# Performance work log

Hardware: AMD Instinct MI355X
Metric: run time of the kernel (lower is better)

## Reference

```python
import jax, jax.numpy as jnp
import numpy as np

EPS = 1e-5

def _bn(x, g, b, m, v):
    # eval-mode batchnorm, NCHW, per-channel params
    inv = g / jnp.sqrt(v + EPS)
    return x * inv[None, :, None, None] + (b - m * inv)[None, :, None, None]

def setup_inputs() -> dict:
    key = jax.random.key(0)
    ks = jax.random.split(key, 16)
    C = 64
    x = jax.random.normal(ks[0], (8, C, 64, 64), dtype=jnp.float32)
    w1 = jax.random.normal(ks[1], (C, C, 1, 1), dtype=jnp.float32) * 0.1
    w2 = jax.random.normal(ks[2], (C, 1, 3, 3), dtype=jnp.float32) * 0.1
    w3 = jax.random.normal(ks[3], (C, C, 1, 1), dtype=jnp.float32) * 0.1
    def bn_params(k):
        k1, k2, k3, k4 = jax.random.split(k, 4)
        return (jax.random.uniform(k1, (C,)) + 0.5,
                jax.random.normal(k2, (C,)) * 0.1,
                jax.random.normal(k3, (C,)) * 0.1,
                jax.random.uniform(k4, (C,)) + 0.5)
    g1, b1, m1, v1 = bn_params(ks[4])
    g2, b2, m2, v2 = bn_params(ks[5])
    g3, b3, m3, v3 = bn_params(ks[6])
    return {"x": x, "w1": w1, "bn1_g": g1, "bn1_b": b1, "bn1_m": m1, "bn1_v": v1,
            "w2": w2, "bn2_g": g2, "bn2_b": b2, "bn2_m": m2, "bn2_v": v2,
            "w3": w3, "bn3_g": g3, "bn3_b": b3, "bn3_m": m3, "bn3_v": v3}

def reference(x, w1, bn1_g, bn1_b, bn1_m, bn1_v,
              w2, bn2_g, bn2_b, bn2_m, bn2_v,
              w3, bn3_g, bn3_b, bn3_m, bn3_v):
    B, c, h, w = x.shape
    N = h * w
    # conv1 (1x1) + BN + ReLU -> V
    v = jnp.einsum('bchw,oc->bohw', x, w1[:, :, 0, 0])
    v = jax.nn.relu(_bn(v, bn1_g, bn1_b, bn1_m, bn1_v))
    # attention over spatial positions: Q=K=x, single head, dim=c
    Q = x.reshape(B, c, N)          # bdn
    V = v.reshape(B, c, N)          # bdm
    scores = jnp.einsum('bdn,bdm->bnm', Q, Q) / (c ** 0.5)  # [B,N,N]
    prob = jax.nn.softmax(scores, axis=-1)
    out = jnp.einsum('bnm,bdm->bdn', prob, V).reshape(B, c, h, w)
    # depthwise conv + BN + ReLU
    out = jax.lax.conv_general_dilated(
        out, w2, window_strides=(1, 1), padding='SAME',
        dimension_numbers=('NCHW', 'OIHW', 'NCHW'), feature_group_count=c)
    out = jax.nn.relu(_bn(out, bn2_g, bn2_b, bn2_m, bn2_v))
    # pointwise conv + BN
    out = jnp.einsum('bchw,oc->bohw', out, w3[:, :, 0, 0])
    out = _bn(out, bn3_g, bn3_b, bn3_m, bn3_v)
    # residual (stride==1 and in_size==out_size)
    return out + x
```

## Files before the change

kernel.cpp:

```cpp
#include <hip/hip_runtime.h>
#include <stdint.h>

typedef __attribute__((ext_vector_type(8)))  short s16x8;
typedef __attribute__((ext_vector_type(16))) float f32x16;

union CvtI4 { int4 i; s16x8 s; };

__device__ __forceinline__ unsigned f2bf(float f) {
    union { float f; unsigned u; } v; v.f = f;
    return (v.u + 0x7fffu + ((v.u >> 16) & 1u)) >> 16;
}

__global__ __launch_bounds__(256) void k_prep(
    const float* __restrict__ x, const float* __restrict__ w1,
    const float* __restrict__ g1, const float* __restrict__ b1,
    const float* __restrict__ m1, const float* __restrict__ v1,
    unsigned short* __restrict__ xT, unsigned short* __restrict__ vbf)
{
    __shared__ float X[64 * 65];
    const int b    = blockIdx.x >> 7;
    const int n0   = ((blockIdx.x >> 1) & 63) << 6;
    const int half = blockIdx.x & 1;
    const int tid  = threadIdx.x;
    const float QS = 0.42466090014400953f;

    {
        const int r = tid >> 6, nn = tid & 63;
        const float* xb = x + (size_t)b * 262144 + n0 + nn;
#pragma unroll
        for (int cc = 0; cc < 16; ++cc) {
            int c = cc * 4 + r;
            X[c * 65 + nn] = xb[(size_t)c * 4096];
        }
    }
    __syncthreads();

    {
        const int n8 = tid >> 3, c8 = tid & 7;
        const int n = (half << 5) + n8;
        unsigned u[4];
#pragma unroll
        for (int j = 0; j < 4; ++j) {
            unsigned lo = f2bf(X[(c8 * 8 + 2 * j) * 65 + n] * QS);
            unsigned hi = f2bf(X[(c8 * 8 + 2 * j + 1) * 65 + n] * QS);
            u[j] = lo | (hi << 16);
        }
        uint4 pk; pk.x = u[0]; pk.y = u[1]; pk.z = u[2]; pk.w = u[3];
        *(uint4*)(xT + (((size_t)((b << 12) + n0 + n)) << 6) + (c8 << 3)) = pk;
    }

    {
        const int n = tid & 63, og = tid >> 6;
        float rX[64];
#pragma unroll
        for (int c = 0; c < 64; ++c) rX[c] = X[c * 65 + n];
        unsigned short* vb = vbf + (((size_t)(b << 6)) << 12) + n0 + n;
#pragma unroll 2
        for (int oo = 0; oo < 8; ++oo) {
            int o = (half << 5) + og * 8 + oo;
            float inv = g1[o] * rsqrtf(v1[o] + 1e-5f);
            float sh  = b1[o] - m1[o] * inv;
            float acc = 0.f;
#pragma unroll
            for (int c = 0; c < 64; ++c) acc = fmaf(w1[o * 64 + c], rX[c], acc);
            vb[(size_t)o << 12] = (unsigned short)f2bf(fmaxf(fmaf(acc, inv, sh), 0.f));
        }
    }
}

__global__ __launch_bounds__(256) void k_attn(
    const unsigned short* __restrict__ xT, const unsigned short* __restrict__ vbf,
    unsigned short* __restrict__ outO, float* __restrict__ outL,
    int tilesPer, int nsplit)
{
    __shared__ __align__(16) unsigned short Klds[64 * 64];
    __shared__ __align__(16) unsigned short Vlds[64 * 64];
    __shared__ __align__(16) unsigned short Plds[64 * 64];
    __shared__ float rsLds[4][32];
    __shared__ float denomT[64];

    const int xcd  = blockIdx.x & 7;
    const int slot = blockIdx.x >> 3;
    const int qgrp = slot & 63;
    const int pair = xcd * nsplit + (slot >> 6);
    const int b = pair & 7;
    const int ms = pair >> 3;

    const int tid = threadIdx.x;
    const int w = tid >> 6, lane = tid & 63;
    const int l31 = lane & 31, half = lane >> 5;
    const int qbase = qgrp << 6;

    outO += (size_t)ms * 2097152u;
    outL += (size_t)ms * 32768u;

    const int s = w & 1;
    const int t = w >> 1;

    s16x8 Bq[4];
    {
        const unsigned short* qr = xT +
            (((size_t)((b << 12) + qbase + (t << 5) + l31)) << 6) + (half << 3);
#pragma unroll
        for (int kk = 0; kk < 4; ++kk) {
            CvtI4 c; c.i = *(const int4*)(qr + (kk << 4));
            Bq[kk] = c.s;
        }
    }

    f32x16 O = {0.f,0.f,0.f,0.f,0.f,0.f,0.f,0.f,0.f,0.f,0.f,0.f,0.f,0.f,0.f,0.f};
    float rs = 0.f;
    const int mt0 = ms * tilesPer;

    for (int mt = 0; mt < tilesPer; ++mt) {
        const int m0 = (mt0 + mt) << 6;
        __syncthreads();
#pragma unroll
        for (int it = 0; it < 2; ++it) {
            int lin = (it << 8) + tid;
            {
                int km = lin >> 3, c4 = lin & 7;
                int4 d = *(const int4*)(xT + (((size_t)((b << 12) + m0 + km)) << 6) + (c4 << 3));
                *(int4*)(Klds + (km << 6) + ((c4 ^ (km & 7)) << 3)) = d;
            }
            {
                int vd = lin >> 3, c8 = lin & 7;
                int4 d = *(const int4*)(vbf + (((size_t)((b << 6) + vd)) << 12) + m0 + (c8 << 3));
                *(int4*)(Vlds + (vd << 6) + ((c8 ^ (vd & 7)) << 3)) = d;
            }
        }
        __syncthreads();

        {
            const int km = (s << 5) + l31;
            s16x8 Ak[4];
#pragma unroll
            for (int kk = 0; kk < 4; ++kk) {
                int pos = ((kk << 1) + half) ^ (km & 7);
                Ak[kk] = *(const s16x8*)(Klds + (km << 6) + (pos << 3));
            }
            f32x16 S = {0.f,0.f,0.f,0.f,0.f,0.f,0.f,0.f,0.f,0.f,0.f,0.f,0.f,0.f,0.f,0.f};
            S = __builtin_amdgcn_mfma_f32_32x32x16_bf16(Ak[0], Bq[0], S, 0, 0, 0);
            S = __builtin_amdgcn_mfma_f32_32x32x16_bf16(Ak[1], Bq[1], S, 0, 0, 0);
            S = __builtin_amdgcn_mfma_f32_32x32x16_bf16(Ak[2], Bq[2], S, 0, 0, 0);
            S = __builtin_amdgcn_mfma_f32_32x32x16_bf16(Ak[3], Bq[3], S, 0, 0, 0);

            const int nrow = (t << 5) + l31;
#pragma unroll
            for (int q = 0; q < 4; ++q) {
                float p0 = __builtin_amdgcn_exp2f(S[4*q+0]);
                float p1 = __builtin_amdgcn_exp2f(S[4*q+1]);
                float p2 = __builtin_amdgcn_exp2f(S[4*q+2]);
                float p3 = __builtin_amdgcn_exp2f(S[4*q+3]);
                rs += (p0 + p1) + (p2 + p3);
                union { float f; unsigned u; } a0, a1, a2, a3;
                a0.f = p0; a1.f = p1; a2.f = p2; a3.f = p3;
                uint2 pk;
                pk.x = ((a0.u + 0x8000u) >> 16) | ((a1.u + 0x8000u) & 0xFFFF0000u);
                pk.y = ((a2.u + 0x8000u) >> 16) | ((a3.u + 0x8000u) & 0xFFFF0000u);
                int c8 = (s << 2) + q;
                *(uint2*)(Plds + (nrow << 6) + ((c8 ^ (nrow & 7)) << 3) + (half << 2)) = pk;
            }
        }
        __syncthreads();

        {
            const int nrow = (t << 5) + l31;
            const int drow = (s << 5) + l31;
#pragma unroll
            for (int ks = 0; ks < 4; ++ks) {
                int c = (ks << 1) + half;
                const s16x8 Ap = *(const s16x8*)(Plds + (nrow << 6) + ((c ^ (nrow & 7)) << 3));
                const s16x8 Bv = *(const s16x8*)(Vlds + (drow << 6) + ((c ^ (drow & 7)) << 3));
                O = __builtin_amdgcn_mfma_f32_32x32x16_bf16(Ap, Bv, O, 0, 0, 0);
            }
        }
    }

    rs += __shfl_xor(rs, 32);
    if (half == 0) rsLds[w][l31] = rs;
    __syncthreads();
    if (tid < 64) {
        int tt = tid >> 5, n = tid & 31;
        denomT[tid] = rsLds[2 * tt][n] + rsLds[2 * tt + 1][n];
    }
    __syncthreads();

    const int nb = (b << 12) + qbase;
    const int n32o = w >> 1, d32 = w & 1;
    if (nsplit == 1) {
#pragma unroll
        for (int r = 0; r < 16; ++r) {
            int nl = (r & 3) + ((r >> 2) << 3) + (half << 2);
            int n = (n32o << 5) + nl;
            float inv = 1.f / denomT[n];
            outO[((size_t)(nb + n) << 6) + (d32 << 5) + l31] = (unsigned short)f2bf(O[r] * inv);
        }
    } else {
#pragma unroll
        for (int r = 0; r < 16; ++r) {
            int nl = (r & 3) + ((r >> 2) << 3) + (half << 2);
            int n = (n32o << 5) + nl;
            outO[((size_t)(nb + n) << 6) + (d32 << 5) + l31] = (unsigned short)f2bf(O[r]);
        }
        if (tid < 64) outL[nb + tid] = denomT[tid];
    }
}

__global__ __launch_bounds__(256) void k_post(
    const unsigned short* __restrict__ Obase, const float* __restrict__ Lbase,
    const float* __restrict__ x,
    const float* __restrict__ w2,
    const float* __restrict__ g2, const float* __restrict__ b2,
    const float* __restrict__ m2, const float* __restrict__ v2,
    const float* __restrict__ w3,
    const float* __restrict__ g3, const float* __restrict__ b3,
    const float* __restrict__ m3, const float* __restrict__ v3,
    float* __restrict__ out, int nsplit, int normalized)
{
    __shared__ float W[3][64 * 66];
    __shared__ float T2[64 * 66];

    const int b = blockIdx.x >> 6;
    const int h = blockIdx.x & 63;
    const int tid = threadIdx.x;

#pragma unroll
    for (int r = 0; r < 3; ++r) {
        int hh = h + r - 1;
        if (hh >= 0 && hh <= 63) {
#pragma unroll
            for (int i = 0; i < 2; ++i) {
                int lin = (i << 8) + tid;
                int w = lin >> 3, cg = lin & 7;
                size_t npos = (size_t)((b << 12) + (hh << 6) + w);
                float acc[8];
#pragma unroll
                for (int j = 0; j < 8; ++j) acc[j] = 0.f;
                float sl = normalized ? 0.f : Lbase[npos];
                const unsigned short* p0 = Obase + (npos << 6) + (cg << 3);
                for (int s = 0; s < nsplit; ++s) {
                    uint4 v = *(const uint4*)(p0 + (size_t)s * 2097152u);
                    union { float f; unsigned u; } t;
                    t.u = v.x << 16;        acc[0] += t.f;
                    t.u = v.x & 0xFFFF0000u; acc[1] += t.f;
                    t.u = v.y << 16;        acc[2] += t.f;
                    t.u = v.y & 0xFFFF0000u; acc[3] += t.f;
                    t.u = v.z << 16;        acc[4] += t.f;
                    t.u = v.z & 0xFFFF0000u; acc[5] += t.f;
                    t.u = v.w << 16;        acc[6] += t.f;
                    t.u = v.w & 0xFFFF0000u; acc[7] += t.f;
                    if (s && !normalized) sl += Lbase[npos + (size_t)s * 32768u];
                }
                float invd = normalized ? 1.f : 1.f / sl;
                float* Wd = &W[r][w * 66 + (cg << 3)];
#pragma unroll
                for (int j = 0; j < 8; ++j) Wd[j] = acc[j] * invd;
            }
        } else {
#pragma unroll
            for (int i = 0; i < 2; ++i) {
                int lin = (i << 8) + tid;
                float* Wd = &W[r][(lin >> 3) * 66 + ((lin & 7) << 3)];
#pragma unroll
                for (int j = 0; j < 8; ++j) Wd[j] = 0.f;
            }
        }
    }
    __syncthreads();

    const int w = tid & 63, cq = tid >> 6;
    float t16[16];
#pragma unroll
    for (int i = 0; i < 16; ++i) t16[i] = 0.f;

#pragma unroll
    for (int ky = 0; ky < 3; ++ky) {
#pragma unroll
        for (int kx = 0; kx < 3; ++kx) {
            int ww = w + kx - 1;
            if (ww < 0 || ww > 63) continue;
            const int k = ky * 3 + kx;
            const float* Wr = &W[ky][ww * 66 + (cq << 4)];
#pragma unroll
            for (int i = 0; i < 4; ++i) {
                float4 a = *(const float4*)(Wr + (i << 2));
                int c = (cq << 4) + (i << 2);
                t16[i * 4 + 0] = fmaf(w2[(c + 0) * 9 + k], a.x, t16[i * 4 + 0]);
                t16[i * 4 + 1] = fmaf(w2[(c + 1) * 9 + k], a.y, t16[i * 4 + 1]);
                t16[i * 4 + 2] = fmaf(w2[(c + 2) * 9 + k], a.z, t16[i * 4 + 2]);
                t16[i * 4 + 3] = fmaf(w2[(c + 3) * 9 + k], a.w, t16[i * 4 + 3]);
            }
        }
    }
#pragma unroll
    for (int i = 0; i < 16; ++i) {
        int c = (cq << 4) + i;
        float inv = g2[c] * rsqrtf(v2[c] + 1e-5f);
        float sh  = b2[c] - m2[c] * inv;
        T2[w * 66 + c] = fmaxf(fmaf(t16[i], inv, sh), 0.f);
    }
    __syncthreads();

    float rT[64];
#pragma unroll
    for (int c4 = 0; c4 < 16; ++c4)
        *(float4*)&rT[c4 << 2] = *(const float4*)&T2[w * 66 + (c4 << 2)];

    const int hw = (h << 6) + w;
#pragma unroll 2
    for (int oo = 0; oo < 16; ++oo) {
        int o = (cq << 4) + oo;
        float inv = g3[o] * rsqrtf(v3[o] + 1e-5f);
        float sh  = b3[o] - m3[o] * inv;
        float acc = 0.f;
#pragma unroll
        for (int c = 0; c < 64; ++c) acc = fmaf(w3[o * 64 + c], rT[c], acc);
        size_t idx = (((size_t)((b << 6) + o)) << 12) + hw;
        out[idx] = fmaf(acc, inv, sh) + x[idx];
    }
}

extern "C" void kernel_launch(void* const* d_in, const int* in_sizes, int n_in,
                              void* d_out, int out_size, void* d_ws, size_t ws_size,
                              hipStream_t stream)
{
    const float* x  = (const float*)d_in[0];
    const float* w1 = (const float*)d_in[1];
    const float* g1 = (const float*)d_in[2];
    const float* b1 = (const float*)d_in[3];
    const float* m1 = (const float*)d_in[4];
    const float* v1 = (const float*)d_in[5];
    const float* w2 = (const float*)d_in[6];
    const float* g2 = (const float*)d_in[7];
    const float* b2 = (const float*)d_in[8];
    const float* m2 = (const float*)d_in[9];
    const float* v2 = (const float*)d_in[10];
    const float* w3 = (const float*)d_in[11];
    const float* g3 = (const float*)d_in[12];
    const float* b3 = (const float*)d_in[13];
    const float* m3 = (const float*)d_in[14];
    const float* v3 = (const float*)d_in[15];
    float* out = (float*)d_out;

    unsigned short* xT  = (unsigned short*)d_ws;
    unsigned short* vbf = xT + (size_t)8 * 4096 * 64;
    unsigned short* Obase = (unsigned short*)((char*)d_ws + (8u << 20));

    const size_t need4 = (8u << 20) + 4u * ((4u << 20) + (128u << 10));
    const size_t need2 = (8u << 20) + 2u * ((4u << 20) + (128u << 10));
    const int nsplit = (ws_size >= need4) ? 4 : (ws_size >= need2 ? 2 : 1);
    float* Lbase = (float*)(Obase + (size_t)nsplit * 2097152u);

    k_prep<<<1024, 256, 0, stream>>>(x, w1, g1, b1, m1, v1, xT, vbf);
    k_attn<<<nsplit * 512, 256, 0, stream>>>(xT, vbf, Obase, Lbase,
                                             64 / nsplit, nsplit);
    k_post<<<512, 256, 0, stream>>>(Obase, Lbase, x, w2, g2, b2, m2, v2,
                                    w3, g3, b3, m3, v3, out, nsplit, nsplit == 1);
}
```

Baseline: 203.2 us.

## Register-prefetch next K/V tile, use v_perm for bf16 packing, cap split at two

The attention loop now loads the next K and V tiles from global memory into registers while the current tile is computed, then writes them to LDS at the start of the next iteration. This hides global load latency behind the MFMA and softmax work. Packing two bf16 values now uses a single byte-permute instruction instead of shift/mask/or. The key-split count is capped at two instead of four, which halves the attention grid, gives each block more tiles to amortise the prefetch, and reduces partial-result merging in the post kernel, at the cost of less parallelism.

```diff
diff --git a/kernel.cpp b/kernel.cpp
--- a/kernel.cpp
+++ b/kernel.cpp
@@ -112,22 +112,40 @@
     float rs = 0.f;
     const int mt0 = ms * tilesPer;
 
+    const int km0 = tid >> 3, c4 = tid & 7;
+    const int km1 = km0 + 32;
+    const size_t kOff0 = (((size_t)((b << 12) + km0)) << 6) + (c4 << 3);
+    const size_t kOff1 = (((size_t)((b << 12) + km1)) << 6) + (c4 << 3);
+    const size_t vOff0 = (((size_t)((b << 6) + km0)) << 12) + (c4 << 3);
+    const size_t vOff1 = (((size_t)((b << 6) + km1)) << 12) + (c4 << 3);
+    unsigned short* kDst0 = Klds + (km0 << 6) + ((c4 ^ (km0 & 7)) << 3);
+    unsigned short* kDst1 = Klds + (km1 << 6) + ((c4 ^ (km1 & 7)) << 3);
+    unsigned short* vDst0 = Vlds + (km0 << 6) + ((c4 ^ (km0 & 7)) << 3);
+    unsigned short* vDst1 = Vlds + (km1 << 6) + ((c4 ^ (km1 & 7)) << 3);
+
+    int4 kpre0, kpre1, vpre0, vpre1;
+    {
+        const size_t m0c = (size_t)(mt0 << 6) << 6;
+        const int m0 = mt0 << 6;
+        kpre0 = *(const int4*)(xT + kOff0 + m0c);
+        kpre1 = *(const int4*)(xT + kOff1 + m0c);
+        vpre0 = *(const int4*)(vbf + vOff0 + m0);
+        vpre1 = *(const int4*)(vbf + vOff1 + m0);
+    }
+
     for (int mt = 0; mt < tilesPer; ++mt) {
-        const int m0 = (mt0 + mt) << 6;
         __syncthreads();
-#pragma unroll
-        for (int it = 0; it < 2; ++it) {
-            int lin = (it << 8) + tid;
-            {
-                int km = lin >> 3, c4 = lin & 7;
-                int4 d = *(const int4*)(xT + (((size_t)((b << 12) + m0 + km)) << 6) + (c4 << 3));
-                *(int4*)(Klds + (km << 6) + ((c4 ^ (km & 7)) << 3)) = d;
-            }
-            {
-                int vd = lin >> 3, c8 = lin & 7;
-                int4 d = *(const int4*)(vbf + (((size_t)((b << 6) + vd)) << 12) + m0 + (c8 << 3));
-                *(int4*)(Vlds + (vd << 6) + ((c8 ^ (vd & 7)) << 3)) = d;
-            }
+        *(int4*)kDst0 = kpre0;
+        *(int4*)kDst1 = kpre1;
+        *(int4*)vDst0 = vpre0;
+        *(int4*)vDst1 = vpre1;
+        if (mt + 1 < tilesPer) {
+            const int m1 = (mt0 + mt + 1) << 6;
+            const size_t m1c = (size_t)m1 << 6;
+            kpre0 = *(const int4*)(xT + kOff0 + m1c);
+            kpre1 = *(const int4*)(xT + kOff1 + m1c);
+            vpre0 = *(const int4*)(vbf + vOff0 + m1);
+            vpre1 = *(const int4*)(vbf + vOff1 + m1);
         }
         __syncthreads();
 
@@ -156,8 +174,8 @@
                 union { float f; unsigned u; } a0, a1, a2, a3;
                 a0.f = p0; a1.f = p1; a2.f = p2; a3.f = p3;
                 uint2 pk;
-                pk.x = ((a0.u + 0x8000u) >> 16) | ((a1.u + 0x8000u) & 0xFFFF0000u);
-                pk.y = ((a2.u + 0x8000u) >> 16) | ((a3.u + 0x8000u) & 0xFFFF0000u);
+                pk.x = __builtin_amdgcn_perm(a1.u + 0x8000u, a0.u + 0x8000u, 0x07060302u);
+                pk.y = __builtin_amdgcn_perm(a3.u + 0x8000u, a2.u + 0x8000u, 0x07060302u);
                 int c8 = (s << 2) + q;
                 *(uint2*)(Plds + (nrow << 6) + ((c8 ^ (nrow & 7)) << 3) + (half << 2)) = pk;
             }
@@ -347,9 +365,8 @@
     unsigned short* vbf = xT + (size_t)8 * 4096 * 64;
     unsigned short* Obase = (unsigned short*)((char*)d_ws + (8u << 20));
 
-    const size_t need4 = (8u << 20) + 4u * ((4u << 20) + (128u << 10));
     const size_t need2 = (8u << 20) + 2u * ((4u << 20) + (128u << 10));
-    const int nsplit = (ws_size >= need4) ? 4 : (ws_size >= need2 ? 2 : 1);
+    const int nsplit = (ws_size >= need2) ? 2 : 1;
     float* Lbase = (float*)(Obase + (size_t)nsplit * 2097152u);
 
     k_prep<<<1024, 256, 0, stream>>>(x, w1, g1, b1, m1, v1, xT, vbf);
```

Result: faster. 198.8 us (-2.2%).

## Warp-specialize attention into QK/softmax and PV waves with double-buffered LDS

Applied to the files above, without the earlier changes.

Replaces the split-KV attention (up to 4 splits plus a merge in k_post) with a single 512-thread block per query tile. Four waves compute QK^T, exp and P while the other four do the PV MFMA on the previous tile, with double-buffered K, V and P in LDS and register prefetch of upcoming tiles. This is meant to overlap the softmax and global loads with the PV matmul and to remove the split partials' write/read traffic and the merge work. The cost is half the grid size (512 blocks), so there is less parallelism across CUs and more LDS per block. It also swaps the bf16 packing to v_perm.

```diff
diff --git a/kernel.cpp b/kernel.cpp
--- a/kernel.cpp
+++ b/kernel.cpp
@@ -68,37 +68,44 @@
     }
 }
 
-__global__ __launch_bounds__(256) void k_attn(
+__global__ __launch_bounds__(512) void k_attn(
     const unsigned short* __restrict__ xT, const unsigned short* __restrict__ vbf,
-    unsigned short* __restrict__ outO, float* __restrict__ outL,
-    int tilesPer, int nsplit)
+    unsigned short* __restrict__ outO)
 {
-    __shared__ __align__(16) unsigned short Klds[64 * 64];
-    __shared__ __align__(16) unsigned short Vlds[64 * 64];
-    __shared__ __align__(16) unsigned short Plds[64 * 64];
+    __shared__ __align__(16) unsigned short Klds[2][64 * 64];
+    __shared__ __align__(16) unsigned short Vlds[2][64 * 64];
+    __shared__ __align__(16) unsigned short Plds[2][64 * 64];
     __shared__ float rsLds[4][32];
     __shared__ float denomT[64];
 
-    const int xcd  = blockIdx.x & 7;
-    const int slot = blockIdx.x >> 3;
-    const int qgrp = slot & 63;
-    const int pair = xcd * nsplit + (slot >> 6);
-    const int b = pair & 7;
-    const int ms = pair >> 3;
-
-    const int tid = threadIdx.x;
+    const int b    = blockIdx.x & 7;
+    const int qgrp = blockIdx.x >> 3;
+    const int tid  = threadIdx.x;
     const int w = tid >> 6, lane = tid & 63;
     const int l31 = lane & 31, half = lane >> 5;
     const int qbase = qgrp << 6;
-
-    outO += (size_t)ms * 2097152u;
-    outL += (size_t)ms * 32768u;
-
-    const int s = w & 1;
-    const int t = w >> 1;
+    const int T = 64;
+
+    const bool isQK = (w < 4);
+    const int wr = isQK ? w : (w - 4);
+    const int s = wr & 1;
+    const int t = wr >> 1;
 
     s16x8 Bq[4];
-    {
+    float rs = 0.f;
+    const int kr0 = (tid & 255) >> 3, c4 = tid & 7;
+    const int kr1 = kr0 + 32;
+    const size_t kOff0 = (((size_t)((b << 12) + kr0)) << 6) + (c4 << 3);
+    const size_t kOff1 = (((size_t)((b << 12) + kr1)) << 6) + (c4 << 3);
+    const int kx0 = (c4 ^ (kr0 & 7)) << 3, kx1 = (c4 ^ (kr1 & 7)) << 3;
+    const size_t vOff0 = (((size_t)((b << 6) + kr0)) << 12) + (c4 << 3);
+    const size_t vOff1 = (((size_t)((b << 6) + kr1)) << 12) + (c4 << 3);
+
+    int4 kpre0, kpre1, vpre0, vpre1;
+
+    f32x16 O = {0.f,0.f,0.f,0.f,0.f,0.f,0.f,0.f,0.f,0.f,0.f,0.f,0.f,0.f,0.f,0.f};
+
+    if (isQK) {
         const unsigned short* qr = xT +
             (((size_t)((b << 12) + qbase + (t << 5) + l31)) << 6) + (half << 3);
 #pragma unroll
@@ -106,79 +113,124 @@
             CvtI4 c; c.i = *(const int4*)(qr + (kk << 4));
             Bq[kk] = c.s;
         }
-    }
-
-    f32x16 O = {0.f,0.f,0.f,0.f,0.f,0.f,0.f,0.f,0.f,0.f,0.f,0.f,0.f,0.f,0.f,0.f};
-    float rs = 0.f;
-    const int mt0 = ms * tilesPer;
-
-    for (int mt = 0; mt < tilesPer; ++mt) {
-        const int m0 = (mt0 + mt) << 6;
-        __syncthreads();
-#pragma unroll
-        for (int it = 0; it < 2; ++it) {
-            int lin = (it << 8) + tid;
+        {
+            int4 a0 = *(const int4*)(xT + kOff0);
+            int4 a1 = *(const int4*)(xT + kOff1);
+            *(int4*)(Klds[0] + (kr0 << 6) + kx0) = a0;
+            *(int4*)(Klds[0] + (kr1 << 6) + kx1) = a1;
+            a0 = *(const int4*)(xT + kOff0 + ((size_t)1 << 12));
+            a1 = *(const int4*)(xT + kOff1 + ((size_t)1 << 12));
+            *(int4*)(Klds[1] + (kr0 << 6) + kx0) = a0;
+            *(int4*)(Klds[1] + (kr1 << 6) + kx1) = a1;
+            kpre0 = *(const int4*)(xT + kOff0 + ((size_t)2 << 12));
+            kpre1 = *(const int4*)(xT + kOff1 + ((size_t)2 << 12));
+        }
+    } else {
+        int4 a0 = *(const int4*)(vbf + vOff0);
+        int4 a1 = *(const int4*)(vbf + vOff1);
+        *(int4*)(Vlds[0] + (kr0 << 6) + kx0) = a0;
+        *(int4*)(Vlds[0] + (kr1 << 6) + kx1) = a1;
+        vpre0 = *(const int4*)(vbf + vOff0 + (1 << 6));
+        vpre1 = *(const int4*)(vbf + vOff1 + (1 << 6));
+    }
+    __syncthreads();
+
+    if (isQK) {
+        const int km = (s << 5) + l31;
+        s16x8 Ak[4];
+#pragma unroll
+        for (int kk = 0; kk < 4; ++kk)
+            Ak[kk] = *(const s16x8*)(Klds[0] + (km << 6) + ((((kk << 1) + half) ^ (km & 7)) << 3));
+        f32x16 S = {0.f,0.f,0.f,0.f,0.f,0.f,0.f,0.f,0.f,0.f,0.f,0.f,0.f,0.f,0.f,0.f};
+        S = __builtin_amdgcn_mfma_f32_32x32x16_bf16(Ak[0], Bq[0], S, 0, 0, 0);
+        S = __builtin_amdgcn_mfma_f32_32x32x16_bf16(Ak[1], Bq[1], S, 0, 0, 0);
+        S = __builtin_amdgcn_mfma_f32_32x32x16_bf16(Ak[2], Bq[2], S, 0, 0, 0);
+        S = __builtin_amdgcn_mfma_f32_32x32x16_bf16(Ak[3], Bq[3], S, 0, 0, 0);
+        const int nrow = (t << 5) + l31;
+#pragma unroll
+        for (int q = 0; q < 4; ++q) {
+            float p0 = __builtin_amdgcn_exp2f(S[4*q+0]);
+            float p1 = __builtin_amdgcn_exp2f(S[4*q+1]);
+            float p2 = __builtin_amdgcn_exp2f(S[4*q+2]);
+            float p3 = __builtin_amdgcn_exp2f(S[4*q+3]);
+            rs += (p0 + p1) + (p2 + p3);
+            union { float f; unsigned u; } a0, a1, a2, a3;
+            a0.f = p0; a1.f = p1; a2.f = p2; a3.f = p3;
+            uint2 pk;
+            pk.x = __builtin_amdgcn_perm(a1.u + 0x8000u, a0.u + 0x8000u, 0x07060302u);
+            pk.y = __builtin_amdgcn_perm(a3.u + 0x8000u, a2.u + 0x8000u, 0x07060302u);
+            int c8 = (s << 2) + q;
+            *(uint2*)(Plds[0] + (nrow << 6) + ((c8 ^ (nrow & 7)) << 3) + (half << 2)) = pk;
+        }
+    }
+    __syncthreads();
+
+    for (int i = 0; i < T; ++i) {
+        if (isQK) {
+            *(int4*)(Klds[i & 1] + (kr0 << 6) + kx0) = kpre0;
+            *(int4*)(Klds[i & 1] + (kr1 << 6) + kx1) = kpre1;
             {
-                int km = lin >> 3, c4 = lin & 7;
-                int4 d = *(const int4*)(xT + (((size_t)((b << 12) + m0 + km)) << 6) + (c4 << 3));
-                *(int4*)(Klds + (km << 6) + ((c4 ^ (km & 7)) << 3)) = d;
-            }
+                size_t tk = (size_t)((i + 3 < T) ? (i + 3) : (T - 1)) << 12;
+                kpre0 = *(const int4*)(xT + kOff0 + tk);
+                kpre1 = *(const int4*)(xT + kOff1 + tk);
+            }
+            if (i + 1 < T) {
+                const int km = (s << 5) + l31;
+                const unsigned short* Kb = Klds[(i + 1) & 1];
+                s16x8 Ak[4];
+#pragma unroll
+                for (int kk = 0; kk < 4; ++kk)
+                    Ak[kk] = *(const s16x8*)(Kb + (km << 6) + ((((kk << 1) + half) ^ (km & 7)) << 3));
+                f32x16 S = {0.f,0.f,0.f,0.f,0.f,0.f,0.f,0.f,0.f,0.f,0.f,0.f,0.f,0.f,0.f,0.f};
+                S = __builtin_amdgcn_mfma_f32_32x32x16_bf16(Ak[0], Bq[0], S, 0, 0, 0);
+                S = __builtin_amdgcn_mfma_f32_32x32x16_bf16(Ak[1], Bq[1], S, 0, 0, 0);
+                S = __builtin_amdgcn_mfma_f32_32x32x16_bf16(Ak[2], Bq[2], S, 0, 0, 0);
+                S = __builtin_amdgcn_mfma_f32_32x32x16_bf16(Ak[3], Bq[3], S, 0, 0, 0);
+                const int nrow = (t << 5) + l31;
+                unsigned short* Pb = Plds[(i + 1) & 1];
+#pragma unroll
+                for (int q = 0; q < 4; ++q) {
+                    float p0 = __builtin_amdgcn_exp2f(S[4*q+0]);
+                    float p1 = __builtin_amdgcn_exp2f(S[4*q+1]);
+                    float p2 = __builtin_amdgcn_exp2f(S[4*q+2]);
+                    float p3 = __builtin_amdgcn_exp2f(S[4*q+3]);
+                    rs += (p0 + p1) + (p2 + p3);
+                    union { float f; unsigned u; } a0, a1, a2, a3;
+                    a0.f = p0; a1.f = p1; a2.f = p2; a3.f = p3;
+                    uint2 pk;
+                    pk.x = __builtin_amdgcn_perm(a1.u + 0x8000u, a0.u + 0x8000u, 0x07060302u);
+                    pk.y = __builtin_amdgcn_perm(a3.u + 0x8000u, a2.u + 0x8000u, 0x07060302u);
+                    int c8 = (s << 2) + q;
+                    *(uint2*)(Pb + (nrow << 6) + ((c8 ^ (nrow & 7)) << 3) + (half << 2)) = pk;
+                }
+            }
+        } else {
+            *(int4*)(Vlds[(i + 1) & 1] + (kr0 << 6) + kx0) = vpre0;
+            *(int4*)(Vlds[(i + 1) & 1] + (kr1 << 6) + kx1) = vpre1;
             {
-                int vd = lin >> 3, c8 = lin & 7;
-                int4 d = *(const int4*)(vbf + (((size_t)((b << 6) + vd)) << 12) + m0 + (c8 << 3));
-                *(int4*)(Vlds + (vd << 6) + ((c8 ^ (vd & 7)) << 3)) = d;
-            }
-        }
-        __syncthreads();
-
-        {
-            const int km = (s << 5) + l31;
-            s16x8 Ak[4];
-#pragma unroll
-            for (int kk = 0; kk < 4; ++kk) {
-                int pos = ((kk << 1) + half) ^ (km & 7);
-                Ak[kk] = *(const s16x8*)(Klds + (km << 6) + (pos << 3));
-            }
-            f32x16 S = {0.f,0.f,0.f,0.f,0.f,0.f,0.f,0.f,0.f,0.f,0.f,0.f,0.f,0.f,0.f,0.f};
-            S = __builtin_amdgcn_mfma_f32_32x32x16_bf16(Ak[0], Bq[0], S, 0, 0, 0);
-            S = __builtin_amdgcn_mfma_f32_32x32x16_bf16(Ak[1], Bq[1], S, 0, 0, 0);
-            S = __builtin_amdgcn_mfma_f32_32x32x16_bf16(Ak[2], Bq[2], S, 0, 0, 0);
-            S = __builtin_amdgcn_mfma_f32_32x32x16_bf16(Ak[3], Bq[3], S, 0, 0, 0);
-
-            const int nrow = (t << 5) + l31;
-#pragma unroll
-            for (int q = 0; q < 4; ++q) {
-                float p0 = __builtin_amdgcn_exp2f(S[4*q+0]);
-                float p1 = __builtin_amdgcn_exp2f(S[4*q+1]);
-                float p2 = __builtin_amdgcn_exp2f(S[4*q+2]);
-                float p3 = __builtin_amdgcn_exp2f(S[4*q+3]);
-                rs += (p0 + p1) + (p2 + p3);
-                union { float f; unsigned u; } a0, a1, a2, a3;
-                a0.f = p0; a1.f = p1; a2.f = p2; a3.f = p3;
-                uint2 pk;
-                pk.x = ((a0.u + 0x8000u) >> 16) | ((a1.u + 0x8000u) & 0xFFFF0000u);
-                pk.y = ((a2.u + 0x8000u) >> 16) | ((a3.u + 0x8000u) & 0xFFFF0000u);
-                int c8 = (s << 2) + q;
-                *(uint2*)(Plds + (nrow << 6) + ((c8 ^ (nrow & 7)) << 3) + (half << 2)) = pk;
-            }
-        }
-        __syncthreads();
-
-        {
+                int tv = ((i + 2 < T) ? (i + 2) : (T - 1)) << 6;
+                vpre0 = *(const int4*)(vbf + vOff0 + tv);
+                vpre1 = *(const int4*)(vbf + vOff1 + tv);
+            }
             const int nrow = (t << 5) + l31;
             const int drow = (s << 5) + l31;
+            const unsigned short* Pb = Plds[i & 1];
+            const unsigned short* Vb = Vlds[i & 1];
 #pragma unroll
             for (int ks = 0; ks < 4; ++ks) {
                 int c = (ks << 1) + half;
-                const s16x8 Ap = *(const s16x8*)(Plds + (nrow << 6) + ((c ^ (nrow & 7)) << 3));
-                const s16x8 Bv = *(const s16x8*)(Vlds + (drow << 6) + ((c ^ (drow & 7)) << 3));
+                const s16x8 Ap = *(const s16x8*)(Pb + (nrow << 6) + ((c ^ (nrow & 7)) << 3));
+                const s16x8 Bv = *(const s16x8*)(Vb + (drow << 6) + ((c ^ (drow & 7)) << 3));
                 O = __builtin_amdgcn_mfma_f32_32x32x16_bf16(Ap, Bv, O, 0, 0, 0);
             }
         }
-    }
-
-    rs += __shfl_xor(rs, 32);
-    if (half == 0) rsLds[w][l31] = rs;
+        __syncthreads();
+    }
+
+    if (isQK) {
+        rs += __shfl_xor(rs, 32);
+        if (half == 0) rsLds[w][l31] = rs;
+    }
     __syncthreads();
     if (tid < 64) {
         int tt = tid >> 5, n = tid & 31;
@@ -186,29 +238,20 @@
     }
     __syncthreads();
 
-    const int nb = (b << 12) + qbase;
-    const int n32o = w >> 1, d32 = w & 1;
-    if (nsplit == 1) {
+    if (!isQK) {
+        const int nb = (b << 12) + qbase;
 #pragma unroll
         for (int r = 0; r < 16; ++r) {
             int nl = (r & 3) + ((r >> 2) << 3) + (half << 2);
-            int n = (n32o << 5) + nl;
+            int n = (t << 5) + nl;
             float inv = 1.f / denomT[n];
-            outO[((size_t)(nb + n) << 6) + (d32 << 5) + l31] = (unsigned short)f2bf(O[r] * inv);
-        }
-    } else {
-#pragma unroll
-        for (int r = 0; r < 16; ++r) {
-            int nl = (r & 3) + ((r >> 2) << 3) + (half << 2);
-            int n = (n32o << 5) + nl;
-            outO[((size_t)(nb + n) << 6) + (d32 << 5) + l31] = (unsigned short)f2bf(O[r]);
-        }
-        if (tid < 64) outL[nb + tid] = denomT[tid];
+            outO[((size_t)(nb + n) << 6) + (s << 5) + l31] = (unsigned short)f2bf(O[r] * inv);
+        }
     }
 }
 
 __global__ __launch_bounds__(256) void k_post(
-    const unsigned short* __restrict__ Obase, const float* __restrict__ Lbase,
+    const unsigned short* __restrict__ Obase,
     const float* __restrict__ x,
     const float* __restrict__ w2,
     const float* __restrict__ g2, const float* __restrict__ b2,
@@ -216,7 +259,7 @@
     const float* __restrict__ w3,
     const float* __restrict__ g3, const float* __restrict__ b3,
     const float* __restrict__ m3, const float* __restrict__ v3,
-    float* __restrict__ out, int nsplit, int normalized)
+    float* __restrict__ out)
 {
     __shared__ float W[3][64 * 66];
     __shared__ float T2[64 * 66];
@@ -234,28 +277,17 @@
                 int lin = (i << 8) + tid;
                 int w = lin >> 3, cg = lin & 7;
                 size_t npos = (size_t)((b << 12) + (hh << 6) + w);
-                float acc[8];
-#pragma unroll
-                for (int j = 0; j < 8; ++j) acc[j] = 0.f;
-                float sl = normalized ? 0.f : Lbase[npos];
-                const unsigned short* p0 = Obase + (npos << 6) + (cg << 3);
-                for (int s = 0; s < nsplit; ++s) {
-                    uint4 v = *(const uint4*)(p0 + (size_t)s * 2097152u);
-                    union { float f; unsigned u; } t;
-                    t.u = v.x << 16;        acc[0] += t.f;
-                    t.u = v.x & 0xFFFF0000u; acc[1] += t.f;
-                    t.u = v.y << 16;        acc[2] += t.f;
-                    t.u = v.y & 0xFFFF0000u; acc[3] += t.f;
-                    t.u = v.z << 16;        acc[4] += t.f;
-                    t.u = v.z & 0xFFFF0000u; acc[5] += t.f;
-                    t.u = v.w << 16;        acc[6] += t.f;
-                    t.u = v.w & 0xFFFF0000u; acc[7] += t.f;
-                    if (s && !normalized) sl += Lbase[npos + (size_t)s * 32768u];
-                }
-                float invd = normalized ? 1.f : 1.f / sl;
+                uint4 v = *(const uint4*)(Obase + (npos << 6) + (cg << 3));
                 float* Wd = &W[r][w * 66 + (cg << 3)];
-#pragma unroll
-                for (int j = 0; j < 8; ++j) Wd[j] = acc[j] * invd;
+                union { float f; unsigned u; } t;
+                t.u = v.x << 16;         Wd[0] = t.f;
+                t.u = v.x & 0xFFFF0000u; Wd[1] = t.f;
+                t.u = v.y << 16;         Wd[2] = t.f;
+                t.u = v.y & 0xFFFF0000u; Wd[3] = t.f;
+                t.u = v.z << 16;         Wd[4] = t.f;
+                t.u = v.z & 0xFFFF0000u; Wd[5] = t.f;
+                t.u = v.w << 16;         Wd[6] = t.f;
+                t.u = v.w & 0xFFFF0000u; Wd[7] = t.f;
             }
         } else {
 #pragma unroll
@@ -347,14 +379,8 @@
     unsigned short* vbf = xT + (size_t)8 * 4096 * 64;
     unsigned short* Obase = (unsigned short*)((char*)d_ws + (8u << 20));
 
-    const size_t need4 = (8u << 20) + 4u * ((4u << 20) + (128u << 10));
-    const size_t need2 = (8u << 20) + 2u * ((4u << 20) + (128u << 10));
-    const int nsplit = (ws_size >= need4) ? 4 : (ws_size >= need2 ? 2 : 1);
-    float* Lbase = (float*)(Obase + (size_t)nsplit * 2097152u);
-
     k_prep<<<1024, 256, 0, stream>>>(x, w1, g1, b1, m1, v1, xT, vbf);
-    k_attn<<<nsplit * 512, 256, 0, stream>>>(xT, vbf, Obase, Lbase,
-                                             64 / nsplit, nsplit);
-    k_post<<<512, 256, 0, stream>>>(Obase, Lbase, x, w2, g2, b2, m2, v2,
-                                    w3, g3, b3, m3, v3, out, nsplit, nsplit == 1);
-}
+    k_attn<<<512, 512, 0, stream>>>(xT, vbf, Obase);
+    k_post<<<512, 256, 0, stream>>>(Obase, x, w2, g2, b2, m2, v2,
+                                    w3, g3, b3, m3, v3, out);
+}
```

New measurement: 192.6 us. 1.05x faster.

## Warp-specialize attention kernel into QK/softmax and PV producer-consumer pipeline

Applied to the files above, without the earlier changes.

The attention kernel now uses 512-thread blocks covering 128 query rows. Four waves compute QK^T and exp into a double-buffered P tile, and four other waves do the P·V MFMAs on the previous tile. K and V tiles are double-buffered in LDS with register prefetch two to three tiles ahead, which cuts the three barriers per tile down to one. The key-split factor drops from 4 to 2, and bf16 packing now uses a single perm instruction. The aim is to overlap the softmax/exp work with the PV matrix multiplies and to hide global-load latency, at the cost of fewer blocks, more LDS and more registers per block.

```diff
diff --git a/kernel.cpp b/kernel.cpp
--- a/kernel.cpp
+++ b/kernel.cpp
@@ -68,84 +68,98 @@
     }
 }
 
-__global__ __launch_bounds__(256) void k_attn(
+__global__ __launch_bounds__(512, 4) void k_attn(
     const unsigned short* __restrict__ xT, const unsigned short* __restrict__ vbf,
     unsigned short* __restrict__ outO, float* __restrict__ outL,
-    int tilesPer, int nsplit)
+    int tilesPer, int normalize)
 {
-    __shared__ __align__(16) unsigned short Klds[64 * 64];
-    __shared__ __align__(16) unsigned short Vlds[64 * 64];
-    __shared__ __align__(16) unsigned short Plds[64 * 64];
-    __shared__ float rsLds[4][32];
-    __shared__ float denomT[64];
-
-    const int xcd  = blockIdx.x & 7;
+    __shared__ __align__(16) unsigned short Klds[2][64 * 64];
+    __shared__ __align__(16) unsigned short Vlds[2][64 * 64];
+    __shared__ __align__(16) unsigned short Plds[2][128 * 64];
+    __shared__ float denomT[128];
+
+    const int b    = blockIdx.x & 7;
     const int slot = blockIdx.x >> 3;
-    const int qgrp = slot & 63;
-    const int pair = xcd * nsplit + (slot >> 6);
-    const int b = pair & 7;
-    const int ms = pair >> 3;
-
-    const int tid = threadIdx.x;
+    const int qgrp = slot & 31;
+    const int ms   = slot >> 5;
+    const int tid  = threadIdx.x;
     const int w = tid >> 6, lane = tid & 63;
     const int l31 = lane & 31, half = lane >> 5;
-    const int qbase = qgrp << 6;
+    const int qbase = qgrp << 7;
 
     outO += (size_t)ms * 2097152u;
     outL += (size_t)ms * 32768u;
-
-    const int s = w & 1;
-    const int t = w >> 1;
+    const int mt0 = ms * tilesPer, mtLast = mt0 + tilesPer - 1;
+
+    const bool isQK = (w < 4);
+    const int wr = isQK ? w : (w - 4);
 
     s16x8 Bq[4];
-    {
+    float rs = 0.f;
+    const int kr0 = (tid & 255) >> 3, c4 = tid & 7;
+    const int kr1 = kr0 + 32;
+    const size_t kOff0 = (((size_t)((b << 12) + kr0)) << 6) + (c4 << 3);
+    const size_t kOff1 = (((size_t)((b << 12) + kr1)) << 6) + (c4 << 3);
+    const int kx0 = (c4 ^ (kr0 & 7)) << 3, kx1 = (c4 ^ (kr1 & 7)) << 3;
+    const size_t vOff0 = (((size_t)((b << 6) + kr0)) << 12) + (c4 << 3);
+    const size_t vOff1 = (((size_t)((b << 6) + kr1)) << 12) + (c4 << 3);
+
+    int4 kpre0, kpre1, vpre0, vpre1;
+
+    f32x16 O0 = {0.f,0.f,0.f,0.f,0.f,0.f,0.f,0.f,0.f,0.f,0.f,0.f,0.f,0.f,0.f,0.f};
+    f32x16 O1 = O0;
+
+    if (isQK) {
         const unsigned short* qr = xT +
-            (((size_t)((b << 12) + qbase + (t << 5) + l31)) << 6) + (half << 3);
+            (((size_t)((b << 12) + qbase + (wr << 5) + l31)) << 6) + (half << 3);
 #pragma unroll
         for (int kk = 0; kk < 4; ++kk) {
             CvtI4 c; c.i = *(const int4*)(qr + (kk << 4));
             Bq[kk] = c.s;
         }
-    }
-
-    f32x16 O = {0.f,0.f,0.f,0.f,0.f,0.f,0.f,0.f,0.f,0.f,0.f,0.f,0.f,0.f,0.f,0.f};
-    float rs = 0.f;
-    const int mt0 = ms * tilesPer;
-
-    for (int mt = 0; mt < tilesPer; ++mt) {
-        const int m0 = (mt0 + mt) << 6;
-        __syncthreads();
-#pragma unroll
-        for (int it = 0; it < 2; ++it) {
-            int lin = (it << 8) + tid;
-            {
-                int km = lin >> 3, c4 = lin & 7;
-                int4 d = *(const int4*)(xT + (((size_t)((b << 12) + m0 + km)) << 6) + (c4 << 3));
-                *(int4*)(Klds + (km << 6) + ((c4 ^ (km & 7)) << 3)) = d;
-            }
-            {
-                int vd = lin >> 3, c8 = lin & 7;
-                int4 d = *(const int4*)(vbf + (((size_t)((b << 6) + vd)) << 12) + m0 + (c8 << 3));
-                *(int4*)(Vlds + (vd << 6) + ((c8 ^ (vd & 7)) << 3)) = d;
-            }
-        }
-        __syncthreads();
-
-        {
-            const int km = (s << 5) + l31;
-            s16x8 Ak[4];
-#pragma unroll
-            for (int kk = 0; kk < 4; ++kk) {
-                int pos = ((kk << 1) + half) ^ (km & 7);
-                Ak[kk] = *(const s16x8*)(Klds + (km << 6) + (pos << 3));
-            }
-            f32x16 S = {0.f,0.f,0.f,0.f,0.f,0.f,0.f,0.f,0.f,0.f,0.f,0.f,0.f,0.f,0.f,0.f};
-            S = __builtin_amdgcn_mfma_f32_32x32x16_bf16(Ak[0], Bq[0], S, 0, 0, 0);
-            S = __builtin_amdgcn_mfma_f32_32x32x16_bf16(Ak[1], Bq[1], S, 0, 0, 0);
-            S = __builtin_amdgcn_mfma_f32_32x32x16_bf16(Ak[2], Bq[2], S, 0, 0, 0);
-            S = __builtin_amdgcn_mfma_f32_32x32x16_bf16(Ak[3], Bq[3], S, 0, 0, 0);
-
-            const int nrow = (t << 5) + l31;
+        int4 a0 = *(const int4*)(xT + kOff0 + ((size_t)mt0 << 12));
+        int4 a1 = *(const int4*)(xT + kOff1 + ((size_t)mt0 << 12));
+        *(int4*)(Klds[0] + (kr0 << 6) + kx0) = a0;
+        *(int4*)(Klds[0] + (kr1 << 6) + kx1) = a1;
+        int t1 = (mt0 + 1 <= mtLast) ? mt0 + 1 : mtLast;
+        a0 = *(const int4*)(xT + kOff0 + ((size_t)t1 << 12));
+        a1 = *(const int4*)(xT + kOff1 + ((size_t)t1 << 12));
+        *(int4*)(Klds[1] + (kr0 << 6) + kx0) = a0;
+        *(int4*)(Klds[1] + (kr1 << 6) + kx1) = a1;
+        int t2 = (mt0 + 2 <= mtLast) ? mt0 + 2 : mtLast;
+        kpre0 = *(const int4*)(xT + kOff0 + ((size_t)t2 << 12));
+        kpre1 = *(const int4*)(xT + kOff1 + ((size_t)t2 << 12));
+    } else {
+        int4 a0 = *(const int4*)(vbf + vOff0 + (mt0 << 6));
+        int4 a1 = *(const int4*)(vbf + vOff1 + (mt0 << 6));
+        *(int4*)(Vlds[0] + (kr0 << 6) + kx0) = a0;
+        *(int4*)(Vlds[0] + (kr1 << 6) + kx1) = a1;
+        int t1 = (mt0 + 1 <= mtLast) ? mt0 + 1 : mtLast;
+        vpre0 = *(const int4*)(vbf + vOff0 + (t1 << 6));
+        vpre1 = *(const int4*)(vbf + vOff1 + (t1 << 6));
+    }
+    __syncthreads();
+
+    auto produceP = [&](int kb, int pb) {
+        const int m0r = l31, m1r = 32 + l31;
+        s16x8 Ak0[4], Ak1[4];
+#pragma unroll
+        for (int kk = 0; kk < 4; ++kk) {
+            Ak0[kk] = *(const s16x8*)(Klds[kb] + (m0r << 6) + ((((kk << 1) + half) ^ (m0r & 7)) << 3));
+            Ak1[kk] = *(const s16x8*)(Klds[kb] + (m1r << 6) + ((((kk << 1) + half) ^ (m1r & 7)) << 3));
+        }
+        f32x16 S0 = {0.f,0.f,0.f,0.f,0.f,0.f,0.f,0.f,0.f,0.f,0.f,0.f,0.f,0.f,0.f,0.f};
+        f32x16 S1 = S0;
+#pragma unroll
+        for (int kk = 0; kk < 4; ++kk) {
+            S0 = __builtin_amdgcn_mfma_f32_32x32x16_bf16(Ak0[kk], Bq[kk], S0, 0, 0, 0);
+            S1 = __builtin_amdgcn_mfma_f32_32x32x16_bf16(Ak1[kk], Bq[kk], S1, 0, 0, 0);
+        }
+        const int nrow = (wr << 5) + l31;
+        unsigned short* Pb = Plds[pb];
+#pragma unroll
+        for (int sgrp = 0; sgrp < 2; ++sgrp) {
+            const f32x16& S = sgrp ? S1 : S0;
 #pragma unroll
             for (int q = 0; q < 4; ++q) {
                 float p0 = __builtin_amdgcn_exp2f(S[4*q+0]);
@@ -156,54 +170,72 @@
                 union { float f; unsigned u; } a0, a1, a2, a3;
                 a0.f = p0; a1.f = p1; a2.f = p2; a3.f = p3;
                 uint2 pk;
-                pk.x = ((a0.u + 0x8000u) >> 16) | ((a1.u + 0x8000u) & 0xFFFF0000u);
-                pk.y = ((a2.u + 0x8000u) >> 16) | ((a3.u + 0x8000u) & 0xFFFF0000u);
-                int c8 = (s << 2) + q;
-                *(uint2*)(Plds + (nrow << 6) + ((c8 ^ (nrow & 7)) << 3) + (half << 2)) = pk;
-            }
-        }
-        __syncthreads();
-
-        {
-            const int nrow = (t << 5) + l31;
-            const int drow = (s << 5) + l31;
+                pk.x = __builtin_amdgcn_perm(a1.u + 0x8000u, a0.u + 0x8000u, 0x07060302u);
+                pk.y = __builtin_amdgcn_perm(a3.u + 0x8000u, a2.u + 0x8000u, 0x07060302u);
+                int c8 = (sgrp << 2) + q;
+                *(uint2*)(Pb + (nrow << 6) + ((c8 ^ (nrow & 7)) << 3) + (half << 2)) = pk;
+            }
+        }
+    };
+
+    if (isQK) produceP(0, 0);
+    __syncthreads();
+
+    for (int i = 0; i < tilesPer; ++i) {
+        if (isQK) {
+            *(int4*)(Klds[i & 1] + (kr0 << 6) + kx0) = kpre0;
+            *(int4*)(Klds[i & 1] + (kr1 << 6) + kx1) = kpre1;
+            {
+                int tk = (mt0 + i + 3 <= mtLast) ? mt0 + i + 3 : mtLast;
+                kpre0 = *(const int4*)(xT + kOff0 + ((size_t)tk << 12));
+                kpre1 = *(const int4*)(xT + kOff1 + ((size_t)tk << 12));
+            }
+            if (i + 1 < tilesPer) produceP((i + 1) & 1, (i + 1) & 1);
+        } else {
+            *(int4*)(Vlds[(i + 1) & 1] + (kr0 << 6) + kx0) = vpre0;
+            *(int4*)(Vlds[(i + 1) & 1] + (kr1 << 6) + kx1) = vpre1;
+            {
+                int tv = (mt0 + i + 2 <= mtLast) ? mt0 + i + 2 : mtLast;
+                vpre0 = *(const int4*)(vbf + vOff0 + (tv << 6));
+                vpre1 = *(const int4*)(vbf + vOff1 + (tv << 6));
+            }
+            const int nrow = (wr << 5) + l31;
+            const int dr0 = l31, dr1 = 32 + l31;
+            const unsigned short* Pb = Plds[i & 1];
+            const unsigned short* Vb = Vlds[i & 1];
 #pragma unroll
             for (int ks = 0; ks < 4; ++ks) {
                 int c = (ks << 1) + half;
-                const s16x8 Ap = *(const s16x8*)(Plds + (nrow << 6) + ((c ^ (nrow & 7)) << 3));
-                const s16x8 Bv = *(const s16x8*)(Vlds + (drow << 6) + ((c ^ (drow & 7)) << 3));
-                O = __builtin_amdgcn_mfma_f32_32x32x16_bf16(Ap, Bv, O, 0, 0, 0);
-            }
-        }
-    }
-
-    rs += __shfl_xor(rs, 32);
-    if (half == 0) rsLds[w][l31] = rs;
-    __syncthreads();
-    if (tid < 64) {
-        int tt = tid >> 5, n = tid & 31;
-        denomT[tid] = rsLds[2 * tt][n] + rsLds[2 * tt + 1][n];
-    }
-    __syncthreads();
+                const s16x8 Ap  = *(const s16x8*)(Pb + (nrow << 6) + ((c ^ (nrow & 7)) << 3));
+                const s16x8 Bv0 = *(const s16x8*)(Vb + (dr0 << 6) + ((c ^ (dr0 & 7)) << 3));
+                const s16x8 Bv1 = *(const s16x8*)(Vb + (dr1 << 6) + ((c ^ (dr1 & 7)) << 3));
+                O0 = __builtin_amdgcn_mfma_f32_32x32x16_bf16(Ap, Bv0, O0, 0, 0, 0);
+                O1 = __builtin_amdgcn_mfma_f32_32x32x16_bf16(Ap, Bv1, O1, 0, 0, 0);
+            }
+        }
+        __syncthreads();
+    }
 
     const int nb = (b << 12) + qbase;
-    const int n32o = w >> 1, d32 = w & 1;
-    if (nsplit == 1) {
+    if (isQK) {
+        rs += __shfl_xor(rs, 32);
+        if (half == 0) {
+            denomT[(wr << 5) + l31] = rs;
+            if (!normalize) outL[nb + (wr << 5) + l31] = rs;
+        }
+    }
+    __syncthreads();
+
+    if (!isQK) {
 #pragma unroll
         for (int r = 0; r < 16; ++r) {
             int nl = (r & 3) + ((r >> 2) << 3) + (half << 2);
-            int n = (n32o << 5) + nl;
-            float inv = 1.f / denomT[n];
-            outO[((size_t)(nb + n) << 6) + (d32 << 5) + l31] = (unsigned short)f2bf(O[r] * inv);
-        }
-    } else {
-#pragma unroll
-        for (int r = 0; r < 16; ++r) {
-            int nl = (r & 3) + ((r >> 2) << 3) + (half << 2);
-            int n = (n32o << 5) + nl;
-            outO[((size_t)(nb + n) << 6) + (d32 << 5) + l31] = (unsigned short)f2bf(O[r]);
-        }
-        if (tid < 64) outL[nb + tid] = denomT[tid];
+            int n = (wr << 5) + nl;
+            float sc = normalize ? (1.f / denomT[n]) : 1.f;
+            unsigned short* row = outO + ((size_t)(nb + n) << 6) + l31;
+            row[0]  = (unsigned short)f2bf(O0[r] * sc);
+            row[32] = (unsigned short)f2bf(O1[r] * sc);
+        }
     }
 }
 
@@ -347,14 +379,13 @@
     unsigned short* vbf = xT + (size_t)8 * 4096 * 64;
     unsigned short* Obase = (unsigned short*)((char*)d_ws + (8u << 20));
 
-    const size_t need4 = (8u << 20) + 4u * ((4u << 20) + (128u << 10));
     const size_t need2 = (8u << 20) + 2u * ((4u << 20) + (128u << 10));
-    const int nsplit = (ws_size >= need4) ? 4 : (ws_size >= need2 ? 2 : 1);
+    const int nsplit = (ws_size >= need2) ? 2 : 1;
     float* Lbase = (float*)(Obase + (size_t)nsplit * 2097152u);
 
     k_prep<<<1024, 256, 0, stream>>>(x, w1, g1, b1, m1, v1, xT, vbf);
-    k_attn<<<nsplit * 512, 256, 0, stream>>>(xT, vbf, Obase, Lbase,
-                                             64 / nsplit, nsplit);
+    k_attn<<<nsplit * 256, 512, 0, stream>>>(xT, vbf, Obase, Lbase,
+                                             64 / nsplit, nsplit == 1);
     k_post<<<512, 256, 0, stream>>>(Obase, Lbase, x, w2, g2, b2, m2, v2,
                                     w3, g3, b3, m3, v3, out, nsplit, nsplit == 1);
 }
```

Result: slower. 259.7 us (+27.8%).
